# Kernel optimization log

Measured on AMD Instinct MI355X. Metric: run time of the kernel, lower is better.

The kernel has to match this reference:

```python
import jax, jax.numpy as jnp
import numpy as np

NUM_BASE = 92
NUM_NOVEL = 40
GAMMA = 2.0
ALPHA = 0.25
DISTIL_FACTOR = 1.0
BSZ, N_DET, DIM_FEAT, DIM_HID, DIM_EMB = 16, 48, 2048, 1024, 512
EMB_HALF = DIM_EMB // 2


def _pair_ids(n):
    # all ordered pairs (i, j), i != j  (trajid2pairid)
    s, o = np.meshgrid(np.arange(n), np.arange(n), indexing='ij')
    m = s != o
    return s[m].astype(np.int32), o[m].astype(np.int32)


def _norm(x, eps=1e-12):
    # F.normalize(dim=-1)
    return x / jnp.maximum(jnp.linalg.norm(x, axis=-1, keepdims=True), eps)


def _sigmoid_focal_loss(logits, targets):
    # torchvision.ops.sigmoid_focal_loss, alpha=0.25, gamma=2, reduction='none'
    p = jax.nn.sigmoid(logits)
    ce = jnp.maximum(logits, 0) - logits * targets + jnp.log1p(jnp.exp(-jnp.abs(logits)))
    p_t = p * targets + (1.0 - p) * (1.0 - targets)
    loss = ce * (1.0 - p_t) ** GAMMA
    a_t = ALPHA * targets + (1.0 - ALPHA) * (1.0 - targets)
    return a_t * loss


def setup_inputs() -> dict:
    key = jax.random.key(0)
    ks = jax.random.split(key, 12)
    sids_np, oids_np = _pair_ids(N_DET)
    P = sids_np.shape[0]  # 2256 pairs per video
    w = lambda k, shape, s=0.02: jax.random.normal(k, shape, dtype=jnp.float32) * s
    return {
        'det_feats': jax.random.normal(ks[0], (BSZ, N_DET, DIM_FEAT), dtype=jnp.float32),
        'traj_embds': jax.random.normal(ks[1], (BSZ, N_DET, EMB_HALF), dtype=jnp.float32),
        'relpos_feats': jax.random.normal(ks[2], (BSZ, P, 12), dtype=jnp.float32),
        'classifier_weights': _norm(jax.random.normal(ks[3], (NUM_BASE, DIM_EMB), dtype=jnp.float32)) / np.sqrt(2.0),
        'W1': w(ks[4], (2 * DIM_FEAT, DIM_HID)), 'b1': jnp.zeros((DIM_HID,), jnp.float32),
        'W2': w(ks[5], (DIM_HID, DIM_HID)), 'b2': jnp.zeros((DIM_HID,), jnp.float32),
        'W3': w(ks[6], (DIM_HID, DIM_EMB)),
        'R1': w(ks[7], (12, 256), 0.1), 'rb1': jnp.zeros((256,), jnp.float32),
        'R2': w(ks[8], (256, DIM_EMB), 0.1),
        'temperature': jnp.full((1,), 0.02, dtype=jnp.float32),
        'labels': jax.random.randint(ks[9], (BSZ, P, 1 + NUM_BASE + NUM_NOVEL), 0, 2, dtype=jnp.int32),
        'sids': jnp.asarray(sids_np),
        'oids': jnp.asarray(oids_np),
    }


def reference(det_feats, traj_embds, relpos_feats, classifier_weights,
              W1, b1, W2, b2, W3, R1, rb1, R2, temperature,
              labels, sids, oids):
    Df = det_feats.shape[-1]
    De = traj_embds.shape[-1]
    # gather subject / object features for all pairs, flatten batch
    s_f = det_feats[:, sids, :].reshape(-1, Df)   # [N, Df]
    o_f = det_feats[:, oids, :].reshape(-1, Df)
    so = jnp.concatenate([s_f, o_f], axis=-1)      # [N, 2*Df]
    # trajpair_proj MLP
    h = jax.nn.relu(so @ W1 + b1)
    h = jax.nn.relu(h @ W2 + b2)
    so_proj = h @ W3                                # [N, dim_emb]
    so_n = _norm(so_proj)
    # relpos branch
    rp = relpos_feats.reshape(-1, relpos_feats.shape[-1])
    re = jax.nn.relu(rp @ R1 + rb1) @ R2
    re = _norm(re)
    combined = _norm(so_n + re)
    logits = (combined @ classifier_weights.T) / temperature  # [N, num_base]
    # cls_loss_on_base
    lab = labels.reshape(-1, 1 + NUM_BASE + NUM_NOVEL).astype(logits.dtype)
    pos_mask = jnp.any(lab[:, 1:1 + NUM_BASE] > 0, axis=-1)
    neg_mask = lab[:, 0] > 0
    lab_base = lab[:, 1:1 + NUM_BASE]
    fl_pos = _sigmoid_focal_loss(logits, lab_base)
    pos_den = jnp.maximum(pos_mask.sum(), 1).astype(logits.dtype) * NUM_BASE
    pos_loss = jnp.sum(fl_pos * pos_mask[:, None]) / pos_den
    fl_neg = _sigmoid_focal_loss(logits, jnp.zeros_like(logits))
    neg_den = jnp.maximum(neg_mask.sum(), 1).astype(logits.dtype) * NUM_BASE
    neg_loss = jnp.sum(fl_neg * neg_mask[:, None]) / neg_den
    # distillation L1 loss
    s_e = traj_embds[:, sids, :].reshape(-1, De)
    o_e = traj_embds[:, oids, :].reshape(-1, De)
    distil_target = jnp.concatenate([s_e, o_e], axis=-1)  # [N, dim_emb]
    distil_loss = jnp.mean(jnp.abs(distil_target - so_proj)) * DISTIL_FACTOR
    total_loss = pos_loss + neg_loss + distil_loss
    return total_loss
```

## Files before the change

kernel.cpp:

```cpp
#include <hip/hip_runtime.h>
#include <math.h>

constexpr int BSZ   = 16;
constexpr int NDET  = 48;
constexpr int PAIRS = NDET * (NDET - 1);
constexpr int ROWS  = BSZ * PAIRS;
constexpr int DF    = 2048;
constexpr int DH    = 1024;
constexpr int DE    = 512;
constexpr int EHALF = 256;
constexpr int NCLS  = 92;
constexpr int NEXT  = DE + 128;
constexpr int LABW  = 1 + 92 + 40;

typedef __attribute__((ext_vector_type(8))) short bf16x8;
typedef __attribute__((ext_vector_type(4))) float f32x4;

__device__ __forceinline__ short f2bf(float f) {
    union { float f; unsigned u; } a; a.f = f;
    unsigned r = a.u + 0x7fffu + ((a.u >> 16) & 1u);
    return (short)(r >> 16);
}
__device__ __forceinline__ float bf2f(short h) {
    union { unsigned u; float f; } x;
    x.u = ((unsigned)(unsigned short)h) << 16;
    return x.f;
}

constexpr int N4DET = BSZ * NDET * DF / 4;
constexpr int N4CWT = 128 * DE / 4;
constexpr int N4W3  = DH * DE / 4;
constexpr int N4R2  = 256 * DE / 4;
constexpr int NCONVB = (N4DET + N4CWT + N4W3 + N4R2) / 256;

struct TransJobs {
    const float* src[5];
    short*       dst[5];
    int K[5], N[5];
    int cum[6];
};

__global__ __launch_bounds__(256) void prep_kernel(
    const float* __restrict__ det, short* __restrict__ det_bf,
    const float* __restrict__ cw, short* __restrict__ cwt,
    const float* __restrict__ W3, short* __restrict__ W3bf,
    const float* __restrict__ R2, short* __restrict__ R2bf,
    TransJobs jobs)
{
    if (blockIdx.x < NCONVB) {
        int i = blockIdx.x * 256 + threadIdx.x;
        const float* src; short* dst; int k;
        if (i < N4DET) { src = det; dst = det_bf; k = i; }
        else if (i < N4DET + N4CWT) {
            k = i - N4DET;
            int n = (k * 4) >> 9;
            short4 o = {0, 0, 0, 0};
            if (n < NCLS) {
                float4 v = ((const float4*)cw)[k];
                o.x = f2bf(v.x); o.y = f2bf(v.y); o.z = f2bf(v.z); o.w = f2bf(v.w);
            }
            ((short4*)cwt)[k] = o;
            return;
        }
        else if (i < N4DET + N4CWT + N4W3) { src = W3; dst = W3bf; k = i - N4DET - N4CWT; }
        else { src = R2; dst = R2bf; k = i - N4DET - N4CWT - N4W3; }
        float4 v = ((const float4*)src)[k];
        short4 o;
        o.x = f2bf(v.x); o.y = f2bf(v.y); o.z = f2bf(v.z); o.w = f2bf(v.w);
        ((short4*)dst)[k] = o;
        return;
    }
    __shared__ float tile[32][33];
    int t = blockIdx.x - NCONVB;
    int j = 0;
    while (t >= jobs.cum[j + 1]) ++j;
    int lt = t - jobs.cum[j];
    int K = jobs.K[j], N = jobs.N[j];
    int nx = N >> 5;
    int ky = lt / nx, nxi = lt - ky * nx;
    int n0 = nxi * 32, k0 = ky * 32;
    const float* src = jobs.src[j];
    short* dst = jobs.dst[j];
    int tx = threadIdx.x & 31, ty = threadIdx.x >> 5;
#pragma unroll
    for (int i = ty; i < 32; i += 8)
        tile[i][tx] = src[(size_t)(k0 + i) * N + n0 + tx];
    __syncthreads();
#pragma unroll
    for (int i = ty; i < 32; i += 8)
        dst[(size_t)(n0 + i) * K + k0 + tx] = f2bf(tile[tx][i]);
}

__device__ __forceinline__ void load16_lds(const void* g, void* l) {
    __builtin_amdgcn_global_load_lds(
        (const __attribute__((address_space(1))) unsigned int*)g,
        (__attribute__((address_space(3))) unsigned int*)l, 16, 0, 0);
}

template <bool BIAS, bool RELU, bool OUTBF16, bool SWIZZLE, bool DUAL>
__global__ __launch_bounds__(256, 4) void mfma_gemm(
    const short* __restrict__ A, const short* __restrict__ Bt,
    const float* __restrict__ bias, void* __restrict__ C,
    int M, int N, int K, int lda, int ldb,
    const short* A2, const short* Bt2, void* C2, int nsplit,
    int K2, int lda2, int ldb2, int N2)
{
    __shared__ __align__(16) char smem_raw[32768];
    short* As = (short*)smem_raw;
    short* Bs = As + 128 * 64;

    int bx, by;
    if (SWIZZLE) {
        int nb  = gridDim.x;
        int gid = blockIdx.y * nb + blockIdx.x;
        int xcd = gid & 7;
        int j   = gid >> 3;
        int rows_per = gridDim.y >> 3;
        int lr  = j / nb;
        bx = j - lr * nb;
        by = xcd * rows_per + lr;
    } else {
        bx = blockIdx.x; by = blockIdx.y;
    }
    if (DUAL && bx >= nsplit) {
        bx -= nsplit; A = A2; Bt = Bt2; C = C2;
        K = K2; lda = lda2; ldb = ldb2; N = N2;
    }
    if (by * 128 >= M) return;

    const int tid  = threadIdx.x;
    const int wave = tid >> 6;
    const int lane = tid & 63;
    const int m0 = by * 128;
    const int n0 = bx * 128;
    const int wm = (wave & 1) * 64;
    const int wn = (wave >> 1) * 64;

    f32x4 acc[4][4] = {};

    const int q  = lane >> 4;
    const int lm = lane & 15;

    for (int k0 = 0; k0 < K; k0 += 64) {
#pragma unroll
        for (int it = 0; it < 4; ++it) {
            int c    = (it & 1) * 256 + tid;
            int half = it >> 1;
            int row  = c >> 2;
            int kk   = (c & 3) * 8 + half * 32;
            int ldsc = half * 4096 + ((it & 1) * 256 + wave * 64) * 8;
            int gm = m0 + row; if (gm >= M) gm = M - 1;
            load16_lds(A + (size_t)gm * lda + k0 + kk, As + ldsc);
            int gn = n0 + row;
            load16_lds(Bt + (size_t)gn * ldb + k0 + kk, Bs + ldsc);
        }
        __syncthreads();

#pragma unroll
        for (int half = 0; half < 2; ++half) {
            const short* Ah = As + half * 4096;
            const short* Bh = Bs + half * 4096;
            bf16x8 af[4], bfr[4];
#pragma unroll
            for (int t = 0; t < 4; ++t) {
                af[t]  = *(const bf16x8*)(Ah + (wm + t * 16 + lm) * 32 + q * 8);
                bfr[t] = *(const bf16x8*)(Bh + (wn + t * 16 + lm) * 32 + q * 8);
            }
#pragma unroll
            for (int tm = 0; tm < 4; ++tm)
#pragma unroll
                for (int tn = 0; tn < 4; ++tn)
                    acc[tm][tn] = __builtin_amdgcn_mfma_f32_16x16x32_bf16(
                        af[tm], bfr[tn], acc[tm][tn], 0, 0, 0);
        }
        __syncthreads();
    }

    if (OUTBF16) {
        float* scratch = (float*)smem_raw + wave * (16 * 68);
#pragma unroll
        for (int tm = 0; tm < 4; ++tm) {
            __syncthreads();
#pragma unroll
            for (int tn = 0; tn < 4; ++tn) {
                float bv = BIAS ? bias[n0 + wn + tn * 16 + lm] : 0.0f;
#pragma unroll
                for (int r = 0; r < 4; ++r) {
                    float v = acc[tm][tn][r] + bv;
                    if (RELU) v = fmaxf(v, 0.0f);
                    scratch[(q * 4 + r) * 68 + tn * 16 + lm] = v;
                }
            }
            __syncthreads();
#pragma unroll
            for (int p = 0; p < 2; ++p) {
                int row16 = (lane >> 3) + p * 8;
                int c0 = (lane & 7) * 8;
                float4 v0 = *(float4*)&scratch[row16 * 68 + c0];
                float4 v1 = *(float4*)&scratch[row16 * 68 + c0 + 4];
                bf16x8 o;
                o[0] = f2bf(v0.x); o[1] = f2bf(v0.y); o[2] = f2bf(v0.z); o[3] = f2bf(v0.w);
                o[4] = f2bf(v1.x); o[5] = f2bf(v1.y); o[6] = f2bf(v1.z); o[7] = f2bf(v1.w);
                int grow = m0 + wm + tm * 16 + row16;
                if (grow < M)
                    *(bf16x8*)((short*)C + (size_t)grow * N + n0 + wn + c0) = o;
            }
        }
    } else {
#pragma unroll
        for (int tm = 0; tm < 4; ++tm)
#pragma unroll
            for (int tn = 0; tn < 4; ++tn) {
                int col = n0 + wn + tn * 16 + lm;
#pragma unroll
                for (int r = 0; r < 4; ++r) {
                    int row = m0 + wm + tm * 16 + q * 4 + r;
                    if (row < M) {
                        float v = acc[tm][tn][r];
                        if (BIAS) v += bias[col];
                        if (RELU) v = fmaxf(v, 0.0f);
                        ((float*)C)[(size_t)row * N + col] = v;
                    }
                }
            }
    }
}

struct GemmJobs {
    const short* A[4]; const short* Bt[4]; short* C[4];
    int M[4], N[4], K[4], lda[4], ldb[4];
    int cum[5];
};

__global__ __launch_bounds__(256, 4) void mfma_gemm_multi(GemmJobs jobs)
{
    __shared__ __align__(16) char smem_raw[32768];
    short* As = (short*)smem_raw;
    short* Bs = As + 128 * 64;

    int bid = blockIdx.x;
    int j = 0;
    while (bid >= jobs.cum[j + 1]) ++j;
    int lt = bid - jobs.cum[j];
    const short* A  = jobs.A[j];
    const short* Bt = jobs.Bt[j];
    short* C = jobs.C[j];
    int M = jobs.M[j], N = jobs.N[j], K = jobs.K[j];
    int lda = jobs.lda[j], ldb = jobs.ldb[j];
    int ncols = N >> 7;
    int by = lt / ncols;
    int bx = lt - by * ncols;

    const int tid  = threadIdx.x;
    const int wave = tid >> 6;
    const int lane = tid & 63;
    const int m0 = by * 128;
    const int n0 = bx * 128;
    const int wm = (wave & 1) * 64;
    const int wn = (wave >> 1) * 64;

    f32x4 acc[4][4] = {};
    const int q  = lane >> 4;
    const int lm = lane & 15;

    for (int k0 = 0; k0 < K; k0 += 64) {
#pragma unroll
        for (int it = 0; it < 4; ++it) {
            int c    = (it & 1) * 256 + tid;
            int half = it >> 1;
            int row  = c >> 2;
            int kk   = (c & 3) * 8 + half * 32;
            int ldsc = half * 4096 + ((it & 1) * 256 + wave * 64) * 8;
            int gm = m0 + row; if (gm >= M) gm = M - 1;
            load16_lds(A + (size_t)gm * lda + k0 + kk, As + ldsc);
            load16_lds(Bt + (size_t)(n0 + row) * ldb + k0 + kk, Bs + ldsc);
        }
        __syncthreads();
#pragma unroll
        for (int half = 0; half < 2; ++half) {
            const short* Ah = As + half * 4096;
            const short* Bh = Bs + half * 4096;
            bf16x8 af[4], bfr[4];
#pragma unroll
            for (int t = 0; t < 4; ++t) {
                af[t]  = *(const bf16x8*)(Ah + (wm + t * 16 + lm) * 32 + q * 8);
                bfr[t] = *(const bf16x8*)(Bh + (wn + t * 16 + lm) * 32 + q * 8);
            }
#pragma unroll
            for (int tm = 0; tm < 4; ++tm)
#pragma unroll
                for (int tn = 0; tn < 4; ++tn)
                    acc[tm][tn] = __builtin_amdgcn_mfma_f32_16x16x32_bf16(
                        af[tm], bfr[tn], acc[tm][tn], 0, 0, 0);
        }
        __syncthreads();
    }

    float* scratch = (float*)smem_raw + wave * (16 * 68);
#pragma unroll
    for (int tm = 0; tm < 4; ++tm) {
        __syncthreads();
#pragma unroll
        for (int tn = 0; tn < 4; ++tn)
#pragma unroll
            for (int r = 0; r < 4; ++r)
                scratch[(q * 4 + r) * 68 + tn * 16 + lm] = acc[tm][tn][r];
        __syncthreads();
#pragma unroll
        for (int p = 0; p < 2; ++p) {
            int row16 = (lane >> 3) + p * 8;
            int c0 = (lane & 7) * 8;
            float4 v0 = *(float4*)&scratch[row16 * 68 + c0];
            float4 v1 = *(float4*)&scratch[row16 * 68 + c0 + 4];
            bf16x8 o;
            o[0] = f2bf(v0.x); o[1] = f2bf(v0.y); o[2] = f2bf(v0.z); o[3] = f2bf(v0.w);
            o[4] = f2bf(v1.x); o[5] = f2bf(v1.y); o[6] = f2bf(v1.z); o[7] = f2bf(v1.w);
            int grow = m0 + wm + tm * 16 + row16;
            if (grow < M)
                *(bf16x8*)(C + (size_t)grow * N + n0 + wn + c0) = o;
        }
    }
}

constexpr int N4UV = BSZ * NDET * 2048 / 4;
__global__ __launch_bounds__(256) void uvmerge_kernel(
    short* __restrict__ UVa, const short* __restrict__ UVb,
    const float* __restrict__ b1)
{
    int i = blockIdx.x * 256 + threadIdx.x;
    if (i >= N4UV) return;
    short4 a = ((const short4*)UVa)[i];
    short4 b = ((const short4*)UVb)[i];
    int col4 = i & 511;
    float4 bb = {0.0f, 0.0f, 0.0f, 0.0f};
    if (col4 < 256) bb = ((const float4*)b1)[col4];
    short4 o;
    o.x = f2bf(bf2f(a.x) + bf2f(b.x) + bb.x);
    o.y = f2bf(bf2f(a.y) + bf2f(b.y) + bb.y);
    o.z = f2bf(bf2f(a.z) + bf2f(b.z) + bb.z);
    o.w = f2bf(bf2f(a.w) + bf2f(b.w) + bb.w);
    ((short4*)UVa)[i] = o;
}

__global__ __launch_bounds__(256) void pairs_rh_kernel(
    const short* __restrict__ UVs,
    const int* __restrict__ sids, const int* __restrict__ oids,
    short* __restrict__ h1,
    const float* __restrict__ rp, const float* __restrict__ R1,
    const float* __restrict__ rb1, short* __restrict__ rh, int b0)
{
    int wave = threadIdx.x >> 6, lane = threadIdx.x & 63;
    int r = blockIdx.x * 4 + wave;
    int b = b0 + r / PAIRS;
    int p = r % PAIRS;

    const bf16x8* us = (const bf16x8*)(UVs + (size_t)(b * NDET + sids[p]) * 2048);
    const bf16x8* uo = (const bf16x8*)(UVs + (size_t)(b * NDET + oids[p]) * 2048 + 1024);
    bf16x8* hrow = (bf16x8*)(h1 + (size_t)r * DH);
#pragma unroll
    for (int i = 0; i < 2; ++i) {
        int idx = lane + i * 64;
        bf16x8 a = us[idx], c = uo[idx];
        bf16x8 h;
#pragma unroll
        for (int e = 0; e < 8; ++e)
            h[e] = f2bf(fmaxf(bf2f(a[e]) + bf2f(c[e]), 0.0f));
        hrow[idx] = h;
    }

    int rg = b0 * PAIRS + r;
    const float* rowp = rp + (size_t)rg * 12;
    float4 acc = ((const float4*)rb1)[lane];
#pragma unroll
    for (int k = 0; k < 12; ++k) {
        float rv = rowp[k];
        float4 w = ((const float4*)(R1 + k * 256))[lane];
        acc.x = fmaf(rv, w.x, acc.x);
        acc.y = fmaf(rv, w.y, acc.y);
        acc.z = fmaf(rv, w.z, acc.z);
        acc.w = fmaf(rv, w.w, acc.w);
    }
    short4 o;
    o.x = f2bf(fmaxf(acc.x, 0.0f));
    o.y = f2bf(fmaxf(acc.y, 0.0f));
    o.z = f2bf(fmaxf(acc.z, 0.0f));
    o.w = f2bf(fmaxf(acc.w, 0.0f));
    ((short4*)(rh + (size_t)r * 256))[lane] = o;
}

__global__ __launch_bounds__(256) void rowprep_focal_kernel(
    const short* __restrict__ so_ext, const short* __restrict__ re_ext,
    const float* __restrict__ traj, const float* __restrict__ temperature,
    const int* __restrict__ sids, const int* __restrict__ oids,
    const int* __restrict__ labels,
    float4* __restrict__ pn, float* __restrict__ dist_arr, int b0)
{
    int wave = threadIdx.x >> 6, lane = threadIdx.x & 63;
    int r = blockIdx.x * 4 + wave;
    int rg = b0 * PAIRS + r;
    int b = b0 + r / PAIRS;
    int p = r % PAIRS;

    const short* srow = so_ext + (size_t)r * NEXT;
    const short* rrow = re_ext + (size_t)r * NEXT;
    bf16x8 sv = *(const bf16x8*)(srow + lane * 8);
    bf16x8 uv = *(const bf16x8*)(rrow + lane * 8);
    float s[8], u[8];
#pragma unroll
    for (int i = 0; i < 8; ++i) { s[i] = bf2f(sv[i]); u[i] = bf2f(uv[i]); }

    const float* tsrc = (lane < 32)
        ? (traj + (size_t)(b * NDET + sids[p]) * EHALF + lane * 8)
        : (traj + (size_t)(b * NDET + oids[p]) * EHALF + (lane - 32) * 8);
    float4 t0 = ((const float4*)tsrc)[0], t1 = ((const float4*)tsrc)[1];
    float t[8] = {t0.x, t0.y, t0.z, t0.w, t1.x, t1.y, t1.z, t1.w};

    float ss = 0.0f, sr = 0.0f, rho = 0.0f, sd = 0.0f;
#pragma unroll
    for (int i = 0; i < 8; ++i) {
        ss  += s[i] * s[i];
        sr  += u[i] * u[i];
        rho += s[i] * u[i];
        sd  += fabsf(t[i] - s[i]);
    }
#pragma unroll
    for (int m = 1; m < 64; m <<= 1) {
        ss  += __shfl_xor(ss, m);
        sr  += __shfl_xor(sr, m);
        rho += __shfl_xor(rho, m);
        sd  += __shfl_xor(sd, m);
    }
    float inv_s = 1.0f / fmaxf(sqrtf(ss), 1e-12f);
    float inv_r = 1.0f / fmaxf(sqrtf(sr), 1e-12f);
    float ncomb = sqrtf(fmaxf(2.0f + 2.0f * rho * inv_s * inv_r, 0.0f));
    float scale = 1.0f / (fmaxf(ncomb, 1e-12f) * temperature[0]);

    float flp = 0.0f, fln = 0.0f, fm = 0.0f;
    size_t labbase = (size_t)rg * LABW;
#pragma unroll
    for (int h = 0; h < 2; ++h) {
        int c = lane + h * 64;
        if (c < NCLS) {
            float l = (bf2f(srow[DE + c]) * inv_s + bf2f(rrow[DE + c]) * inv_r) * scale;
            int tl = labels[labbase + 1 + c];
            if (tl > 0) fm = 1.0f;
            float tf = (float)tl;
            float pr = 1.0f / (1.0f + expf(-l));
            float lg = log1pf(expf(-fabsf(l)));
            float ce = fmaxf(l, 0.0f) - l * tf + lg;
            float pt = pr * tf + (1.0f - pr) * (1.0f - tf);
            float om = 1.0f - pt;
            float at = 0.25f * tf + 0.75f * (1.0f - tf);
            flp += at * ce * om * om;
            float ce0 = fmaxf(l, 0.0f) + lg;
            fln += 0.75f * ce0 * pr * pr;
        }
    }
#pragma unroll
    for (int m = 1; m < 64; m <<= 1) {
        flp += __shfl_xor(flp, m);
        fln += __shfl_xor(fln, m);
        fm  += __shfl_xor(fm, m);
    }
    if (lane == 0) {
        int posf = (fm > 0.5f) ? 1 : 0;
        int negf = (labels[labbase] > 0) ? 1 : 0;
        pn[rg] = make_float4(posf ? flp : 0.0f, negf ? fln : 0.0f, 0.0f,
                             (float)(posf + 2 * negf));
        dist_arr[rg] = sd;
    }
}

struct RedRec { double sp, sn, sd; int cp, cn; };
constexpr int RED1 = 64;
constexpr int ROWS_PER_RED = ROWS / RED1;

__global__ __launch_bounds__(256) void reduce1_kernel(
    const float4* __restrict__ pn, const float* __restrict__ dist_arr,
    RedRec* __restrict__ scratch)
{
    int tid = threadIdx.x;
    int base = blockIdx.x * ROWS_PER_RED;
    double sp = 0.0, sn = 0.0, sd = 0.0;
    int cp = 0, cn = 0;
    for (int i = tid; i < ROWS_PER_RED; i += 256) {
        float4 v = pn[base + i];
        sp += (double)v.x; sn += (double)v.y; sd += (double)dist_arr[base + i];
        int f = (int)v.w;
        cp += f & 1; cn += (f >> 1) & 1;
    }
    __shared__ double A[256], B[256], C[256];
    __shared__ int I[256], J[256];
    A[tid] = sp; B[tid] = sn; C[tid] = sd; I[tid] = cp; J[tid] = cn;
    __syncthreads();
    for (int st = 128; st > 0; st >>= 1) {
        if (tid < st) { A[tid] += A[tid + st]; B[tid] += B[tid + st]; C[tid] += C[tid + st];
                        I[tid] += I[tid + st]; J[tid] += J[tid + st]; }
        __syncthreads();
    }
    if (tid == 0) {
        RedRec rec; rec.sp = A[0]; rec.sn = B[0]; rec.sd = C[0];
        rec.cp = I[0]; rec.cn = J[0];
        scratch[blockIdx.x] = rec;
    }
}

__global__ __launch_bounds__(64) void reduce2_kernel(
    const RedRec* __restrict__ scratch, float* __restrict__ out)
{
    int lane = threadIdx.x;
    RedRec rec = scratch[lane];
    double sp = rec.sp, sn = rec.sn, sd = rec.sd;
    int cp = rec.cp, cn = rec.cn;
#pragma unroll
    for (int m = 1; m < 64; m <<= 1) {
        sp += __shfl_xor(sp, m);
        sn += __shfl_xor(sn, m);
        sd += __shfl_xor(sd, m);
        cp += __shfl_xor(cp, m);
        cn += __shfl_xor(cn, m);
    }
    if (lane == 0) {
        int cpv = cp < 1 ? 1 : cp;
        int cnv = cn < 1 ? 1 : cn;
        out[0] = (float)(sp / ((double)cpv * NCLS) +
                         sn / ((double)cnv * NCLS) +
                         sd / ((double)ROWS * DE));
    }
}

static inline int pad8(int x) { return (x + 7) & ~7; }

extern "C" void kernel_launch(void* const* d_in, const int* in_sizes, int n_in,
                              void* d_out, int out_size, void* d_ws, size_t ws_size,
                              hipStream_t stream)
{
    const float* det    = (const float*)d_in[0];
    const float* traj   = (const float*)d_in[1];
    const float* relpos = (const float*)d_in[2];
    const float* cw     = (const float*)d_in[3];
    const float* W1     = (const float*)d_in[4];
    const float* b1     = (const float*)d_in[5];
    const float* W2     = (const float*)d_in[6];
    const float* b2     = (const float*)d_in[7];
    const float* W3     = (const float*)d_in[8];
    const float* R1     = (const float*)d_in[9];
    const float* rb1    = (const float*)d_in[10];
    const float* R2     = (const float*)d_in[11];
    const float* temp   = (const float*)d_in[12];
    const int*   labels = (const int*)d_in[13];
    const int*   sids   = (const int*)d_in[14];
    const int*   oids   = (const int*)d_in[15];
    float* out = (float*)d_out;

    char* ws = (char*)d_ws;
    size_t off = 0;
    auto carve = [&](size_t bytes) -> char* {
        char* p = ws + off;
        off = (off + bytes + 255) & ~(size_t)255;
        return p;
    };
    float4* pn       = (float4*)carve((size_t)ROWS * 16);
    float*  dist_arr = (float*)carve((size_t)ROWS * 4);
    short*  det_bf   = (short*)carve((size_t)BSZ * NDET * DF * 2);
    short*  W1t      = (short*)carve((size_t)2048 * 2048 * 2);
    short*  W2t      = (short*)carve((size_t)DH * DH * 2);
    short*  W3t      = (short*)carve((size_t)NEXT * DH * 2);
    short*  R2t      = (short*)carve((size_t)NEXT * 256 * 2);
    short*  cwt      = (short*)carve((size_t)128 * DE * 2);
    short*  W3bf     = (short*)carve((size_t)DH * DE * 2);
    short*  R2bf     = (short*)carve((size_t)256 * DE * 2);
    short*  UVa      = (short*)carve((size_t)BSZ * NDET * 2048 * 2);
    short*  UVb      = (short*)carve((size_t)BSZ * NDET * 2048 * 2);
    RedRec* red_scratch = (RedRec*)carve((size_t)RED1 * sizeof(RedRec));
    size_t fixed_off = off;

    int b_ch = 1;
    for (int cand : {16, 8, 4, 2, 1}) {
        size_t rows  = (size_t)cand * PAIRS;
        size_t bytes = fixed_off + rows * 2048 + 256 + rows * 2048 + 256
                     + rows * 512 + 256 + rows * 1280 + 256;
        if (bytes <= ws_size) { b_ch = cand; break; }
    }
    const int chunk_rows = b_ch * PAIRS;
    const int n_chunks = BSZ / b_ch;
    char* reg1 = carve((size_t)chunk_rows * 2048);
    char* reg2 = carve((size_t)chunk_rows * 2048);
    char* reg3 = carve((size_t)chunk_rows * 512);
    char* reg4 = carve((size_t)chunk_rows * 1280);

    short* h1     = (short*)reg1;
    short* h2     = (short*)reg2;
    short* so_ext = (short*)reg1;
    short* rh     = (short*)reg3;
    short* re_ext = (short*)reg4;

    TransJobs tj;
    tj.src[0] = W1;                    tj.dst[0] = W1t;                   tj.K[0] = DF;  tj.N[0] = DH;
    tj.src[1] = W1 + (size_t)DF * DH;  tj.dst[1] = W1t + (size_t)DH * DF; tj.K[1] = DF;  tj.N[1] = DH;
    tj.src[2] = W2;                    tj.dst[2] = W2t;                   tj.K[2] = DH;  tj.N[2] = DH;
    tj.src[3] = W3;                    tj.dst[3] = W3t;                   tj.K[3] = DH;  tj.N[3] = DE;
    tj.src[4] = R2;                    tj.dst[4] = R2t;                   tj.K[4] = 256; tj.N[4] = DE;
    tj.cum[0] = 0;
    for (int i = 0; i < 5; ++i)
        tj.cum[i + 1] = tj.cum[i] + (tj.K[i] / 32) * (tj.N[i] / 32);
    prep_kernel<<<NCONVB + tj.cum[5], 256, 0, stream>>>(
        det, det_bf, cw, cwt, W3, W3bf, R2, R2bf, tj);

    GemmJobs gj;
    gj.A[0] = det_bf;        gj.Bt[0] = W1t;        gj.C[0] = UVa;
    gj.M[0] = BSZ * NDET;    gj.N[0] = 2048;        gj.K[0] = 1024;
    gj.lda[0] = 2048;        gj.ldb[0] = 2048;
    gj.A[1] = det_bf + 1024; gj.Bt[1] = W1t + 1024; gj.C[1] = UVb;
    gj.M[1] = BSZ * NDET;    gj.N[1] = 2048;        gj.K[1] = 1024;
    gj.lda[1] = 2048;        gj.ldb[1] = 2048;
    gj.A[2] = cwt;           gj.Bt[2] = W3bf;       gj.C[2] = W3t + (size_t)512 * DH;
    gj.M[2] = 128;           gj.N[2] = 1024;        gj.K[2] = 512;
    gj.lda[2] = 512;         gj.ldb[2] = 512;
    gj.A[3] = cwt;           gj.Bt[3] = R2bf;       gj.C[3] = R2t + (size_t)512 * 256;
    gj.M[3] = 128;           gj.N[3] = 256;         gj.K[3] = 512;
    gj.lda[3] = 512;         gj.ldb[3] = 512;
    gj.cum[0] = 0;
    for (int i = 0; i < 4; ++i)
        gj.cum[i + 1] = gj.cum[i] + (gj.N[i] / 128) * ((gj.M[i] + 127) / 128);
    mfma_gemm_multi<<<gj.cum[4], 256, 0, stream>>>(gj);

    uvmerge_kernel<<<(N4UV + 255) / 256, 256, 0, stream>>>(UVa, UVb, b1);

    const int mg  = (chunk_rows + 127) / 128;
    const int mgp = pad8(mg);

    for (int c = 0; c < n_chunks; ++c) {
        int b0 = c * b_ch;

        pairs_rh_kernel<<<chunk_rows / 4, 256, 0, stream>>>(
            UVa, sids, oids, h1, relpos, R1, rb1, rh, b0);

        mfma_gemm<true, true, true, true, false>
            <<<dim3(DH / 128, mgp), 256, 0, stream>>>(
            h1, W2t, b2, h2, chunk_rows, DH, DH, DH, DH,
            nullptr, nullptr, nullptr, 0, 0, 0, 0, 0);

        mfma_gemm<false, false, true, true, true>
            <<<dim3(10, mgp), 256, 0, stream>>>(
            h2, W3t, nullptr, so_ext, chunk_rows, NEXT, DH, DH, DH,
            rh, R2t, re_ext, 5, 256, 256, 256, NEXT);

        rowprep_focal_kernel<<<chunk_rows / 4, 256, 0, stream>>>(
            so_ext, re_ext, traj, temp, sids, oids, labels, pn, dist_arr, b0);
    }

    reduce1_kernel<<<RED1, 256, 0, stream>>>(pn, dist_arr, red_scratch);
    reduce2_kernel<<<1, 64, 0, stream>>>(red_scratch, out);
}
```

Baseline: 372.7 us.

## Replace 128x128 GEMM with 256x256 double-buffered, swizzled, phase-pipelined MFMA kernel

Swaps the per-chunk W2 and W3/R2 GEMMs to a new 512-thread kernel with 256x256 tiles, XOR-swizzled LDS layout, double-buffered global-to-LDS prefetch two k-steps ahead, and four interleaved compute phases using setprio. The larger tiles raise arithmetic intensity per LDS load, and the prefetching is meant to overlap memory traffic with MFMA work. W3t/R2t are padded to 768 rows so the N=640 output fits 256-wide tiles, which wastes some compute on padding columns. The XCD swizzle from the old kernel is dropped.

```diff
diff --git a/kernel.cpp b/kernel.cpp
--- a/kernel.cpp
+++ b/kernel.cpp
@@ -11,6 +11,7 @@
 constexpr int EHALF = 256;
 constexpr int NCLS  = 92;
 constexpr int NEXT  = DE + 128;
+constexpr int NPAD  = 768;
 constexpr int LABW  = 1 + 92 + 40;
 
 typedef __attribute__((ext_vector_type(8))) short bf16x8;
@@ -97,132 +98,195 @@
         (__attribute__((address_space(3))) unsigned int*)l, 16, 0, 0);
 }
 
-template <bool BIAS, bool RELU, bool OUTBF16, bool SWIZZLE, bool DUAL>
-__global__ __launch_bounds__(256, 4) void mfma_gemm(
+#define MFMA16 __builtin_amdgcn_mfma_f32_16x16x32_bf16
+
+template <bool BIAS, bool RELU, bool DUAL>
+__global__ __launch_bounds__(512, 2) void gemm256(
     const short* __restrict__ A, const short* __restrict__ Bt,
-    const float* __restrict__ bias, void* __restrict__ C,
-    int M, int N, int K, int lda, int ldb,
-    const short* A2, const short* Bt2, void* C2, int nsplit,
-    int K2, int lda2, int ldb2, int N2)
-{
-    __shared__ __align__(16) char smem_raw[32768];
-    short* As = (short*)smem_raw;
-    short* Bs = As + 128 * 64;
-
-    int bx, by;
-    if (SWIZZLE) {
-        int nb  = gridDim.x;
-        int gid = blockIdx.y * nb + blockIdx.x;
-        int xcd = gid & 7;
-        int j   = gid >> 3;
-        int rows_per = gridDim.y >> 3;
-        int lr  = j / nb;
-        bx = j - lr * nb;
-        by = xcd * rows_per + lr;
-    } else {
-        bx = blockIdx.x; by = blockIdx.y;
-    }
-    if (DUAL && bx >= nsplit) {
-        bx -= nsplit; A = A2; Bt = Bt2; C = C2;
-        K = K2; lda = lda2; ldb = ldb2; N = N2;
-    }
-    if (by * 128 >= M) return;
+    const float* __restrict__ bias, short* __restrict__ C,
+    int M, int NV, int K, int lda, int ldb, int ntn, int nsplit,
+    const short* A2, const short* Bt2, short* C2,
+    int M2, int NV2, int K2, int lda2, int ldb2, int ntn2)
+{
+    __shared__ __align__(16) short smem[2 * 32768];
+
+    int bid = blockIdx.x;
+    if (DUAL && bid >= nsplit) {
+        bid -= nsplit;
+        A = A2; Bt = Bt2; C = C2;
+        M = M2; NV = NV2; K = K2; lda = lda2; ldb = ldb2; ntn = ntn2;
+    }
+    const int by = bid / ntn;
+    const int bx = bid - by * ntn;
+    const int m0 = by * 256;
+    const int n0 = bx * 256;
 
     const int tid  = threadIdx.x;
-    const int wave = tid >> 6;
+    const int wid  = tid >> 6;
     const int lane = tid & 63;
-    const int m0 = by * 128;
-    const int n0 = bx * 128;
-    const int wm = (wave & 1) * 64;
-    const int wn = (wave >> 1) * 64;
-
-    f32x4 acc[4][4] = {};
-
+    const int wr = wid >> 2;
+    const int wc = wid & 3;
     const int q  = lane >> 4;
     const int lm = lane & 15;
 
-    for (int k0 = 0; k0 < K; k0 += 64) {
-#pragma unroll
-        for (int it = 0; it < 4; ++it) {
-            int c    = (it & 1) * 256 + tid;
-            int half = it >> 1;
-            int row  = c >> 2;
-            int kk   = (c & 3) * 8 + half * 32;
-            int ldsc = half * 4096 + ((it & 1) * 256 + wave * 64) * 8;
-            int gm = m0 + row; if (gm >= M) gm = M - 1;
-            load16_lds(A + (size_t)gm * lda + k0 + kk, As + ldsc);
-            int gn = n0 + row;
-            load16_lds(Bt + (size_t)gn * ldb + k0 + kk, Bs + ldsc);
-        }
-        __syncthreads();
-
-#pragma unroll
-        for (int half = 0; half < 2; ++half) {
-            const short* Ah = As + half * 4096;
-            const short* Bh = Bs + half * 4096;
-            bf16x8 af[4], bfr[4];
-#pragma unroll
-            for (int t = 0; t < 4; ++t) {
-                af[t]  = *(const bf16x8*)(Ah + (wm + t * 16 + lm) * 32 + q * 8);
-                bfr[t] = *(const bf16x8*)(Bh + (wn + t * 16 + lm) * 32 + q * 8);
+    const int rowoff = wid * 8 + ((tid & 63) >> 3);
+    const int cs8    = ((tid & 7) ^ ((tid >> 3) & 7)) * 8;
+    const int kc0 = ((q)     ^ (lm & 7)) * 8;
+    const int kc1 = ((4 + q) ^ (lm & 7)) * 8;
+    const int NT  = K >> 6;
+    const int Mm1 = M - 1;
+
+    auto stA = [&](int buf, int r0, int kt) {
+        int gm = m0 + r0 + rowoff; if (gm > Mm1) gm = Mm1;
+        load16_lds(A + (size_t)gm * lda + kt * 64 + cs8,
+                   smem + buf * 32768 + (r0 + wid * 8) * 64);
+    };
+    auto stB = [&](int buf, int r0, int kt) {
+        int gn = n0 + r0 + rowoff;
+        load16_lds(Bt + (size_t)gn * ldb + kt * 64 + cs8,
+                   smem + buf * 32768 + 16384 + (r0 + wid * 8) * 64);
+    };
+
+    stA(0, 0, 0);   stA(0, 64, 0);
+    stB(0, 0, 0);   stB(0, 64, 0);
+    stB(0, 128, 0); stB(0, 192, 0);
+    stA(0, 128, 0); stA(0, 192, 0);
+    if (NT > 1) {
+        stA(1, 0, 1);   stA(1, 64, 1);
+        stB(1, 0, 1);   stB(1, 64, 1);
+        stB(1, 128, 1); stB(1, 192, 1);
+        asm volatile("s_waitcnt vmcnt(6)" ::: "memory");
+    } else {
+        asm volatile("s_waitcnt vmcnt(0)" ::: "memory");
+    }
+    __builtin_amdgcn_s_barrier();
+
+    f32x4 acc[8][4] = {};
+    bf16x8 af[4][2], bq0[2][2], bq1[2][2];
+
+    for (int t = 0; t < NT; ++t) {
+        const short* Ab = smem + (t & 1) * 32768;
+        const short* Bb = Ab + 16384;
+        const int bufc = t & 1, bufn = bufc ^ 1;
+        const bool s1 = (t + 1 < NT);
+        const bool s2 = (t + 2 < NT);
+
+#pragma unroll
+        for (int i = 0; i < 4; ++i) {
+            const short* r = Ab + ((i * 2 + wr) * 16 + lm) * 64;
+            af[i][0] = *(const bf16x8*)(r + kc0);
+            af[i][1] = *(const bf16x8*)(r + kc1);
+        }
+#pragma unroll
+        for (int j = 0; j < 2; ++j) {
+            const short* r = Bb + ((j * 4 + wc) * 16 + lm) * 64;
+            bq0[j][0] = *(const bf16x8*)(r + kc0);
+            bq0[j][1] = *(const bf16x8*)(r + kc1);
+        }
+        if (s1) { stA(bufn, 128, t + 1); stA(bufn, 192, t + 1); }
+        __builtin_amdgcn_s_barrier();
+        asm volatile("s_waitcnt lgkmcnt(0)");
+        __builtin_amdgcn_s_setprio(1);
+#pragma unroll
+        for (int i = 0; i < 4; ++i)
+#pragma unroll
+            for (int j = 0; j < 2; ++j) {
+                acc[i][j] = MFMA16(af[i][0], bq0[j][0], acc[i][j], 0, 0, 0);
+                acc[i][j] = MFMA16(af[i][1], bq0[j][1], acc[i][j], 0, 0, 0);
             }
-#pragma unroll
-            for (int tm = 0; tm < 4; ++tm)
-#pragma unroll
-                for (int tn = 0; tn < 4; ++tn)
-                    acc[tm][tn] = __builtin_amdgcn_mfma_f32_16x16x32_bf16(
-                        af[tm], bfr[tn], acc[tm][tn], 0, 0, 0);
-        }
-        __syncthreads();
-    }
-
-    if (OUTBF16) {
-        float* scratch = (float*)smem_raw + wave * (16 * 68);
-#pragma unroll
-        for (int tm = 0; tm < 4; ++tm) {
-            __syncthreads();
-#pragma unroll
-            for (int tn = 0; tn < 4; ++tn) {
-                float bv = BIAS ? bias[n0 + wn + tn * 16 + lm] : 0.0f;
-#pragma unroll
-                for (int r = 0; r < 4; ++r) {
-                    float v = acc[tm][tn][r] + bv;
-                    if (RELU) v = fmaxf(v, 0.0f);
-                    scratch[(q * 4 + r) * 68 + tn * 16 + lm] = v;
-                }
+        __builtin_amdgcn_s_setprio(0);
+        __builtin_amdgcn_s_barrier();
+
+#pragma unroll
+        for (int j = 0; j < 2; ++j) {
+            const short* r = Bb + (((j + 2) * 4 + wc) * 16 + lm) * 64;
+            bq1[j][0] = *(const bf16x8*)(r + kc0);
+            bq1[j][1] = *(const bf16x8*)(r + kc1);
+        }
+        if (s2) { stA(bufc, 0, t + 2); stA(bufc, 64, t + 2); }
+        __builtin_amdgcn_s_barrier();
+        asm volatile("s_waitcnt lgkmcnt(0)");
+        __builtin_amdgcn_s_setprio(1);
+#pragma unroll
+        for (int i = 0; i < 4; ++i)
+#pragma unroll
+            for (int j = 0; j < 2; ++j) {
+                acc[i][j + 2] = MFMA16(af[i][0], bq1[j][0], acc[i][j + 2], 0, 0, 0);
+                acc[i][j + 2] = MFMA16(af[i][1], bq1[j][1], acc[i][j + 2], 0, 0, 0);
             }
-            __syncthreads();
-#pragma unroll
-            for (int p = 0; p < 2; ++p) {
-                int row16 = (lane >> 3) + p * 8;
-                int c0 = (lane & 7) * 8;
+        __builtin_amdgcn_s_setprio(0);
+        __builtin_amdgcn_s_barrier();
+
+#pragma unroll
+        for (int i = 0; i < 4; ++i) {
+            const short* r = Ab + (((i + 4) * 2 + wr) * 16 + lm) * 64;
+            af[i][0] = *(const bf16x8*)(r + kc0);
+            af[i][1] = *(const bf16x8*)(r + kc1);
+        }
+        if (s2) { stB(bufc, 0, t + 2); stB(bufc, 64, t + 2); }
+        __builtin_amdgcn_s_barrier();
+        asm volatile("s_waitcnt lgkmcnt(0)");
+        __builtin_amdgcn_s_setprio(1);
+#pragma unroll
+        for (int i = 0; i < 4; ++i)
+#pragma unroll
+            for (int j = 0; j < 2; ++j) {
+                acc[i + 4][j] = MFMA16(af[i][0], bq0[j][0], acc[i + 4][j], 0, 0, 0);
+                acc[i + 4][j] = MFMA16(af[i][1], bq0[j][1], acc[i + 4][j], 0, 0, 0);
+            }
+        __builtin_amdgcn_s_setprio(0);
+        __builtin_amdgcn_s_barrier();
+
+        if (s2) { stB(bufc, 128, t + 2); stB(bufc, 192, t + 2); }
+        if (s2)      asm volatile("s_waitcnt vmcnt(6)" ::: "memory");
+        else if (s1) asm volatile("s_waitcnt vmcnt(0)" ::: "memory");
+        __builtin_amdgcn_s_barrier();
+        __builtin_amdgcn_s_setprio(1);
+#pragma unroll
+        for (int i = 0; i < 4; ++i)
+#pragma unroll
+            for (int j = 0; j < 2; ++j) {
+                acc[i + 4][j + 2] = MFMA16(af[i][0], bq1[j][0], acc[i + 4][j + 2], 0, 0, 0);
+                acc[i + 4][j + 2] = MFMA16(af[i][1], bq1[j][1], acc[i + 4][j + 2], 0, 0, 0);
+            }
+        __builtin_amdgcn_s_setprio(0);
+        __builtin_amdgcn_s_barrier();
+    }
+
+    float bv[4] = {0.0f, 0.0f, 0.0f, 0.0f};
+    if (BIAS) {
+#pragma unroll
+        for (int fn = 0; fn < 4; ++fn)
+            bv[fn] = bias[n0 + fn * 64 + wc * 16 + lm];
+    }
+    float* scratch = (float*)smem + wid * (16 * 68);
+    const int c0   = (lane & 7) * 8;
+    const int gcol = n0 + (c0 >> 4) * 64 + wc * 16 + (c0 & 8);
+#pragma unroll
+    for (int fm = 0; fm < 8; ++fm) {
+#pragma unroll
+        for (int fn = 0; fn < 4; ++fn)
+#pragma unroll
+            for (int r = 0; r < 4; ++r) {
+                float v = acc[fm][fn][r] + bv[fn];
+                if (RELU) v = fmaxf(v, 0.0f);
+                scratch[(q * 4 + r) * 68 + fn * 16 + lm] = v;
+            }
+#pragma unroll
+        for (int p = 0; p < 2; ++p) {
+            int row16 = (lane >> 3) + p * 8;
+            int grow  = m0 + (fm * 2 + wr) * 16 + row16;
+            if (grow < M && gcol < NV) {
                 float4 v0 = *(float4*)&scratch[row16 * 68 + c0];
                 float4 v1 = *(float4*)&scratch[row16 * 68 + c0 + 4];
                 bf16x8 o;
-                o[0] = f2bf(v0.x); o[1] = f2bf(v0.y); o[2] = f2bf(v0.z); o[3] = f2bf(v0.w);
-                o[4] = f2bf(v1.x); o[5] = f2bf(v1.y); o[6] = f2bf(v1.z); o[7] = f2bf(v1.w);
-                int grow = m0 + wm + tm * 16 + row16;
-                if (grow < M)
-                    *(bf16x8*)((short*)C + (size_t)grow * N + n0 + wn + c0) = o;
+                o[0] = f2bf(v0.x); o[1] = f2bf(v0.y);
+                o[2] = f2bf(v0.z); o[3] = f2bf(v0.w);
+                o[4] = f2bf(v1.x); o[5] = f2bf(v1.y);
+                o[6] = f2bf(v1.z); o[7] = f2bf(v1.w);
+                *(bf16x8*)(C + (size_t)grow * NV + gcol) = o;
             }
         }
-    } else {
-#pragma unroll
-        for (int tm = 0; tm < 4; ++tm)
-#pragma unroll
-            for (int tn = 0; tn < 4; ++tn) {
-                int col = n0 + wn + tn * 16 + lm;
-#pragma unroll
-                for (int r = 0; r < 4; ++r) {
-                    int row = m0 + wm + tm * 16 + q * 4 + r;
-                    if (row < M) {
-                        float v = acc[tm][tn][r];
-                        if (BIAS) v += bias[col];
-                        if (RELU) v = fmaxf(v, 0.0f);
-                        ((float*)C)[(size_t)row * N + col] = v;
-                    }
-                }
-            }
     }
 }
 
@@ -290,8 +354,7 @@
             for (int tm = 0; tm < 4; ++tm)
 #pragma unroll
                 for (int tn = 0; tn < 4; ++tn)
-                    acc[tm][tn] = __builtin_amdgcn_mfma_f32_16x16x32_bf16(
-                        af[tm], bfr[tn], acc[tm][tn], 0, 0, 0);
+                    acc[tm][tn] = MFMA16(af[tm], bfr[tn], acc[tm][tn], 0, 0, 0);
         }
         __syncthreads();
     }
@@ -528,8 +591,6 @@
                          sd / ((double)ROWS * DE));
     }
 }
-
-static inline int pad8(int x) { return (x + 7) & ~7; }
 
 extern "C" void kernel_launch(void* const* d_in, const int* in_sizes, int n_in,
                               void* d_out, int out_size, void* d_ws, size_t ws_size,
@@ -565,8 +626,8 @@
     short*  det_bf   = (short*)carve((size_t)BSZ * NDET * DF * 2);
     short*  W1t      = (short*)carve((size_t)2048 * 2048 * 2);
     short*  W2t      = (short*)carve((size_t)DH * DH * 2);
-    short*  W3t      = (short*)carve((size_t)NEXT * DH * 2);
-    short*  R2t      = (short*)carve((size_t)NEXT * 256 * 2);
+    short*  W3t      = (short*)carve((size_t)NPAD * DH * 2);
+    short*  R2t      = (short*)carve((size_t)NPAD * 256 * 2);
     short*  cwt      = (short*)carve((size_t)128 * DE * 2);
     short*  W3bf     = (short*)carve((size_t)DH * DE * 2);
     short*  R2bf     = (short*)carve((size_t)256 * DE * 2);
@@ -627,8 +688,7 @@
 
     uvmerge_kernel<<<(N4UV + 255) / 256, 256, 0, stream>>>(UVa, UVb, b1);
 
-    const int mg  = (chunk_rows + 127) / 128;
-    const int mgp = pad8(mg);
+    const int mt = (chunk_rows + 255) / 256;
 
     for (int c = 0; c < n_chunks; ++c) {
         int b0 = c * b_ch;
@@ -636,15 +696,13 @@
         pairs_rh_kernel<<<chunk_rows / 4, 256, 0, stream>>>(
             UVa, sids, oids, h1, relpos, R1, rb1, rh, b0);
 
-        mfma_gemm<true, true, true, true, false>
-            <<<dim3(DH / 128, mgp), 256, 0, stream>>>(
-            h1, W2t, b2, h2, chunk_rows, DH, DH, DH, DH,
-            nullptr, nullptr, nullptr, 0, 0, 0, 0, 0);
-
-        mfma_gemm<false, false, true, true, true>
-            <<<dim3(10, mgp), 256, 0, stream>>>(
-            h2, W3t, nullptr, so_ext, chunk_rows, NEXT, DH, DH, DH,
-            rh, R2t, re_ext, 5, 256, 256, 256, NEXT);
+        gemm256<true, true, false><<<mt * 4, 512, 0, stream>>>(
+            h1, W2t, b2, h2, chunk_rows, DH, DH, DH, DH, 4, 0,
+            nullptr, nullptr, nullptr, 0, 0, 0, 0, 0, 0);
+
+        gemm256<false, false, true><<<mt * 6, 512, 0, stream>>>(
+            h2, W3t, nullptr, so_ext, chunk_rows, NEXT, DH, DH, DH, 3, mt * 3,
+            rh, R2t, re_ext, chunk_rows, NEXT, 256, 256, 256, 3);
 
         rowprep_focal_kernel<<<chunk_rows / 4, 256, 0, stream>>>(
             so_ext, re_ext, traj, temp, sids, oids, labels, pn, dist_arr, b0);
```

Result: slower. 397.6 us (+6.7%).

## Fuse pair gather and ReLU into the W2 GEMM A-operand load

Applied to the files above, without the earlier changes.

Removes materialization of h1 (gathered subject/object UV sum with ReLU) by building the A tile inside a new GEMM kernel from sids/oids-indexed rows of UV, with only relpos projection left in a separate kernel. This saves writing and rereading a chunk_rows x 1024 bf16 buffer per chunk. In exchange, A loads become synchronous register loads plus ALU conversion inside the K loop instead of async global_load_lds, and each UV row is re-read by all 8 N-column blocks, so occupancy and latency hiding may suffer.

```diff
diff --git a/kernel.cpp b/kernel.cpp
--- a/kernel.cpp
+++ b/kernel.cpp
@@ -97,6 +97,8 @@
         (__attribute__((address_space(3))) unsigned int*)l, 16, 0, 0);
 }
 
+#define MFMA16 __builtin_amdgcn_mfma_f32_16x16x32_bf16
+
 template <bool BIAS, bool RELU, bool OUTBF16, bool SWIZZLE, bool DUAL>
 __global__ __launch_bounds__(256, 4) void mfma_gemm(
     const short* __restrict__ A, const short* __restrict__ Bt,
@@ -170,8 +172,7 @@
             for (int tm = 0; tm < 4; ++tm)
 #pragma unroll
                 for (int tn = 0; tn < 4; ++tn)
-                    acc[tm][tn] = __builtin_amdgcn_mfma_f32_16x16x32_bf16(
-                        af[tm], bfr[tn], acc[tm][tn], 0, 0, 0);
+                    acc[tm][tn] = MFMA16(af[tm], bfr[tn], acc[tm][tn], 0, 0, 0);
         }
         __syncthreads();
     }
@@ -226,6 +227,127 @@
     }
 }
 
+__global__ __launch_bounds__(256, 3) void gemm_h2f(
+    const short* __restrict__ UV,
+    const int* __restrict__ sids, const int* __restrict__ oids,
+    const short* __restrict__ Bt, const float* __restrict__ bias,
+    short* __restrict__ C, int M, int rowbase)
+{
+    __shared__ __align__(16) char smem_raw[32768];
+    short* As = (short*)smem_raw;
+    short* Bs = As + 128 * 64;
+
+    int nb  = gridDim.x;
+    int gid = blockIdx.y * nb + blockIdx.x;
+    int xcd = gid & 7;
+    int j   = gid >> 3;
+    int rows_per = gridDim.y >> 3;
+    int lr  = j / nb;
+    int bx = j - lr * nb;
+    int by = xcd * rows_per + lr;
+    if (by * 128 >= M) return;
+
+    const int tid  = threadIdx.x;
+    const int wave = tid >> 6;
+    const int lane = tid & 63;
+    const int m0 = by * 128;
+    const int n0 = bx * 128;
+    const int wm = (wave & 1) * 64;
+    const int wn = (wave >> 1) * 64;
+
+    const int cq = tid & 3;
+    int lr0 = m0 + (tid >> 2); if (lr0 >= M) lr0 = M - 1;
+    int lr1 = lr0 + 64;        if (lr1 >= M) lr1 = M - 1;
+    int rg0 = rowbase + lr0, rg1 = rowbase + lr1;
+    int b0 = rg0 / PAIRS, p0 = rg0 - b0 * PAIRS;
+    int b1 = rg1 / PAIRS, p1 = rg1 - b1 * PAIRS;
+    const short* u0 = UV + (size_t)(b0 * NDET + sids[p0]) * 2048;
+    const short* v0 = UV + (size_t)(b0 * NDET + oids[p0]) * 2048 + 1024;
+    const short* u1 = UV + (size_t)(b1 * NDET + sids[p1]) * 2048;
+    const short* v1 = UV + (size_t)(b1 * NDET + oids[p1]) * 2048 + 1024;
+
+    f32x4 acc[4][4] = {};
+    const int q  = lane >> 4;
+    const int lm = lane & 15;
+
+    for (int k0 = 0; k0 < DH; k0 += 64) {
+#pragma unroll
+        for (int it = 0; it < 4; ++it) {
+            int c    = (it & 1) * 256 + tid;
+            int half = it >> 1;
+            int row  = c >> 2;
+            int kk   = (c & 3) * 8 + half * 32;
+            int ldsc = half * 4096 + ((it & 1) * 256 + wave * 64) * 8;
+            load16_lds(Bt + (size_t)(n0 + row) * DH + k0 + kk, Bs + ldsc);
+        }
+        int ka = k0 + cq * 8;
+        bf16x8 ua0 = *(const bf16x8*)(u0 + ka),      va0 = *(const bf16x8*)(v0 + ka);
+        bf16x8 ua1 = *(const bf16x8*)(u1 + ka),      va1 = *(const bf16x8*)(v1 + ka);
+        bf16x8 ub0 = *(const bf16x8*)(u0 + ka + 32), vb0 = *(const bf16x8*)(v0 + ka + 32);
+        bf16x8 ub1 = *(const bf16x8*)(u1 + ka + 32), vb1 = *(const bf16x8*)(v1 + ka + 32);
+        bf16x8 w0, w1, w2, w3;
+#pragma unroll
+        for (int e = 0; e < 8; ++e) {
+            w0[e] = f2bf(fmaxf(bf2f(ua0[e]) + bf2f(va0[e]), 0.0f));
+            w1[e] = f2bf(fmaxf(bf2f(ua1[e]) + bf2f(va1[e]), 0.0f));
+            w2[e] = f2bf(fmaxf(bf2f(ub0[e]) + bf2f(vb0[e]), 0.0f));
+            w3[e] = f2bf(fmaxf(bf2f(ub1[e]) + bf2f(vb1[e]), 0.0f));
+        }
+        *(bf16x8*)(As + tid * 8)                = w0;
+        *(bf16x8*)(As + (256 + tid) * 8)        = w1;
+        *(bf16x8*)(As + 4096 + tid * 8)         = w2;
+        *(bf16x8*)(As + 4096 + (256 + tid) * 8) = w3;
+        __syncthreads();
+
+#pragma unroll
+        for (int half = 0; half < 2; ++half) {
+            const short* Ah = As + half * 4096;
+            const short* Bh = Bs + half * 4096;
+            bf16x8 af[4], bfr[4];
+#pragma unroll
+            for (int t = 0; t < 4; ++t) {
+                af[t]  = *(const bf16x8*)(Ah + (wm + t * 16 + lm) * 32 + q * 8);
+                bfr[t] = *(const bf16x8*)(Bh + (wn + t * 16 + lm) * 32 + q * 8);
+            }
+#pragma unroll
+            for (int tm = 0; tm < 4; ++tm)
+#pragma unroll
+                for (int tn = 0; tn < 4; ++tn)
+                    acc[tm][tn] = MFMA16(af[tm], bfr[tn], acc[tm][tn], 0, 0, 0);
+        }
+        __syncthreads();
+    }
+
+    float* scratch = (float*)smem_raw + wave * (16 * 68);
+#pragma unroll
+    for (int tm = 0; tm < 4; ++tm) {
+        __syncthreads();
+#pragma unroll
+        for (int tn = 0; tn < 4; ++tn) {
+            float bv = bias[n0 + wn + tn * 16 + lm];
+#pragma unroll
+            for (int r = 0; r < 4; ++r) {
+                float v = fmaxf(acc[tm][tn][r] + bv, 0.0f);
+                scratch[(q * 4 + r) * 68 + tn * 16 + lm] = v;
+            }
+        }
+        __syncthreads();
+#pragma unroll
+        for (int p = 0; p < 2; ++p) {
+            int row16 = (lane >> 3) + p * 8;
+            int c0 = (lane & 7) * 8;
+            float4 x0 = *(float4*)&scratch[row16 * 68 + c0];
+            float4 x1 = *(float4*)&scratch[row16 * 68 + c0 + 4];
+            bf16x8 o;
+            o[0] = f2bf(x0.x); o[1] = f2bf(x0.y); o[2] = f2bf(x0.z); o[3] = f2bf(x0.w);
+            o[4] = f2bf(x1.x); o[5] = f2bf(x1.y); o[6] = f2bf(x1.z); o[7] = f2bf(x1.w);
+            int grow = m0 + wm + tm * 16 + row16;
+            if (grow < M)
+                *(bf16x8*)(C + (size_t)grow * DH + n0 + wn + c0) = o;
+        }
+    }
+}
+
 struct GemmJobs {
     const short* A[4]; const short* Bt[4]; short* C[4];
     int M[4], N[4], K[4], lda[4], ldb[4];
@@ -290,8 +412,7 @@
             for (int tm = 0; tm < 4; ++tm)
 #pragma unroll
                 for (int tn = 0; tn < 4; ++tn)
-                    acc[tm][tn] = __builtin_amdgcn_mfma_f32_16x16x32_bf16(
-                        af[tm], bfr[tn], acc[tm][tn], 0, 0, 0);
+                    acc[tm][tn] = MFMA16(af[tm], bfr[tn], acc[tm][tn], 0, 0, 0);
         }
         __syncthreads();
     }
@@ -342,33 +463,14 @@
     ((short4*)UVa)[i] = o;
 }
 
-__global__ __launch_bounds__(256) void pairs_rh_kernel(
-    const short* __restrict__ UVs,
-    const int* __restrict__ sids, const int* __restrict__ oids,
-    short* __restrict__ h1,
+__global__ __launch_bounds__(256) void rh_kernel(
     const float* __restrict__ rp, const float* __restrict__ R1,
     const float* __restrict__ rb1, short* __restrict__ rh, int b0)
 {
     int wave = threadIdx.x >> 6, lane = threadIdx.x & 63;
     int r = blockIdx.x * 4 + wave;
-    int b = b0 + r / PAIRS;
-    int p = r % PAIRS;
-
-    const bf16x8* us = (const bf16x8*)(UVs + (size_t)(b * NDET + sids[p]) * 2048);
-    const bf16x8* uo = (const bf16x8*)(UVs + (size_t)(b * NDET + oids[p]) * 2048 + 1024);
-    bf16x8* hrow = (bf16x8*)(h1 + (size_t)r * DH);
-#pragma unroll
-    for (int i = 0; i < 2; ++i) {
-        int idx = lane + i * 64;
-        bf16x8 a = us[idx], c = uo[idx];
-        bf16x8 h;
-#pragma unroll
-        for (int e = 0; e < 8; ++e)
-            h[e] = f2bf(fmaxf(bf2f(a[e]) + bf2f(c[e]), 0.0f));
-        hrow[idx] = h;
-    }
-
     int rg = b0 * PAIRS + r;
+
     const float* rowp = rp + (size_t)rg * 12;
     float4 acc = ((const float4*)rb1)[lane];
 #pragma unroll
@@ -589,7 +691,6 @@
     char* reg3 = carve((size_t)chunk_rows * 512);
     char* reg4 = carve((size_t)chunk_rows * 1280);
 
-    short* h1     = (short*)reg1;
     short* h2     = (short*)reg2;
     short* so_ext = (short*)reg1;
     short* rh     = (short*)reg3;
@@ -633,13 +734,11 @@
     for (int c = 0; c < n_chunks; ++c) {
         int b0 = c * b_ch;
 
-        pairs_rh_kernel<<<chunk_rows / 4, 256, 0, stream>>>(
-            UVa, sids, oids, h1, relpos, R1, rb1, rh, b0);
-
-        mfma_gemm<true, true, true, true, false>
-            <<<dim3(DH / 128, mgp), 256, 0, stream>>>(
-            h1, W2t, b2, h2, chunk_rows, DH, DH, DH, DH,
-            nullptr, nullptr, nullptr, 0, 0, 0, 0, 0);
+        rh_kernel<<<chunk_rows / 4, 256, 0, stream>>>(
+            relpos, R1, rb1, rh, b0);
+
+        gemm_h2f<<<dim3(DH / 128, mgp), 256, 0, stream>>>(
+            UVa, sids, oids, W2t, b2, h2, chunk_rows, b0 * PAIRS);
 
         mfma_gemm<false, false, true, true, true>
             <<<dim3(10, mgp), 256, 0, stream>>>(
```

After: 385.7 us. 1.03x slower.
